# Performance work log

Measured on AMD Instinct MI355X. Metric: run time of the kernel, lower is better.

The kernel has to match this reference:

```python
import jax, jax.numpy as jnp
import numpy as np

B, S, D, H = 2, 2048, 2048, 16
HD = D // H  # 128 head dim


def setup_inputs() -> dict:
    key = jax.random.key(0)
    k1, k2, k3 = jax.random.split(key, 3)
    x = jax.random.normal(k1, (B, S, D), dtype=jnp.float32)
    w_qkv = jax.random.normal(k2, (3 * D, D), dtype=jnp.float32) * 0.02
    w_out = jax.random.normal(k3, (D, D), dtype=jnp.float32) * 0.02
    # complex-like RoPE table: freqs_cis[s, j] = exp(i * s * theta^{-2j/hd})
    theta = 10000.0
    inv_freq = 1.0 / (theta ** (jnp.arange(0, HD, 2, dtype=jnp.float32) / HD))  # [HD/2]
    t = jnp.arange(S, dtype=jnp.float32)
    freqs = jnp.outer(t, inv_freq)  # [S, HD/2]
    return {"x": x, "w_qkv": w_qkv, "w_out": w_out,
            "freqs_cos": jnp.cos(freqs), "freqs_sin": jnp.sin(freqs)}


def _apply_rope(t, cos, sin):
    # t: [b, s, h, hd]; adjacent pairs treated as complex (real, imag)
    b, s, h, hd = t.shape
    tr = t.reshape(b, s, h, hd // 2, 2)
    re, im = tr[..., 0], tr[..., 1]
    c = cos[None, :, None, :]  # [1, s, 1, hd/2]
    sn = sin[None, :, None, :]
    out_re = re * c - im * sn
    out_im = re * sn + im * c
    return jnp.stack([out_re, out_im], axis=-1).reshape(b, s, h, hd)


def reference(x, w_qkv, w_out, freqs_cos, freqs_sin):
    b, s, d = x.shape
    qkv = x @ w_qkv.T  # [b, s, 3d]
    q, k, v = jnp.split(qkv, 3, axis=-1)
    q = q.reshape(b, s, H, HD)
    k = k.reshape(b, s, H, HD)
    v = v.reshape(b, s, H, HD)
    q = _apply_rope(q, freqs_cos, freqs_sin)
    k = _apply_rope(k, freqs_cos, freqs_sin)
    # causal SDPA
    scale = 1.0 / jnp.sqrt(jnp.asarray(HD, dtype=x.dtype))
    scores = jnp.einsum("bqhd,bkhd->bhqk", q, k) * scale  # [b, h, s, s]
    causal = jnp.tril(jnp.ones((s, s), dtype=bool))
    scores = jnp.where(causal[None, None], scores, jnp.finfo(scores.dtype).min)
    attn = jax.nn.softmax(scores, axis=-1)
    out = jnp.einsum("bhqk,bkhd->bqhd", attn, v).reshape(b, s, d)
    return out @ w_out.T
```

## Files before the change

### kernel.cpp

```cpp
#include <hip/hip_runtime.h>
#include <hip/hip_bf16.h>
#include <stdint.h>

#define S_ 2048
#define D_ 2048
#define H_ 16
#define HD_ 128

typedef __bf16 bf16x8 __attribute__((ext_vector_type(8)));
typedef float f32x4 __attribute__((ext_vector_type(4)));
typedef unsigned short ushort_t;
typedef ushort_t us4 __attribute__((ext_vector_type(4)));

__device__ __forceinline__ float bf2f(ushort_t u) {
  union { float f; uint32_t i; } x; x.i = ((uint32_t)u) << 16; return x.f;
}
__device__ __forceinline__ ushort_t f2bf(float f) {
  union { float f; uint32_t i; } x; x.f = f;
  uint32_t r = x.i + 0x7fffu + ((x.i >> 16) & 1u);
  return (ushort_t)(r >> 16);
}

__device__ __forceinline__ void async_copy16(const void* g, void* l) {
  __builtin_amdgcn_global_load_lds(
      (const __attribute__((address_space(1))) unsigned int*)g,
      (__attribute__((address_space(3))) unsigned int*)l, 16, 0, 0);
}

__device__ __forceinline__ void store_val(float* p, float v) { *p = v; }
__device__ __forceinline__ void store_val(ushort_t* p, float v) { *p = f2bf(v); }

__global__ __launch_bounds__(256) void cvt_f32_bf16(const float* __restrict__ in,
                                                    ushort_t* __restrict__ out,
                                                    int n4) {
  int i = blockIdx.x * 256 + threadIdx.x;
  if (i >= n4) return;
  const float4 v = ((const float4*)in)[i];
  us4 o;
  o.x = f2bf(v.x); o.y = f2bf(v.y); o.z = f2bf(v.z); o.w = f2bf(v.w);
  ((us4*)out)[i] = o;
}

template <typename OutT>
__global__ __launch_bounds__(256) void gemm_bt(const ushort_t* __restrict__ A,
                                               const ushort_t* __restrict__ Bm,
                                               OutT* __restrict__ C,
                                               int M, int N, int K) {
  __shared__ __align__(16) ushort_t As[128 * 32];
  __shared__ __align__(16) ushort_t Bs[128 * 32];
  const int tid = threadIdx.x;
  const int wave = tid >> 6, lane = tid & 63;
  const int quad = lane >> 4, l16 = lane & 15;
  const int bm = blockIdx.y * 128, bn = blockIdx.x * 128;
  const int wm = (wave >> 1) * 64, wn = (wave & 1) * 64;

  f32x4 acc[4][4] = {};

  const int c0 = wave * 2, c1 = c0 + 1;
  const int srow = lane >> 2;
  const int scol = (lane & 3) * 8;
  const ushort_t* gA0 = A + (size_t)(bm + c0 * 16 + srow) * K + scol;
  const ushort_t* gA1 = A + (size_t)(bm + c1 * 16 + srow) * K + scol;
  const ushort_t* gB0 = Bm + (size_t)(bn + c0 * 16 + srow) * K + scol;
  const ushort_t* gB1 = Bm + (size_t)(bn + c1 * 16 + srow) * K + scol;
  ushort_t* lA0 = As + c0 * 512;
  ushort_t* lA1 = As + c1 * 512;
  ushort_t* lB0 = Bs + c0 * 512;
  ushort_t* lB1 = Bs + c1 * 512;

  for (int k0 = 0; k0 < K; k0 += 32) {
    __syncthreads();
    async_copy16(gA0 + k0, lA0);
    async_copy16(gA1 + k0, lA1);
    async_copy16(gB0 + k0, lB0);
    async_copy16(gB1 + k0, lB1);
    __syncthreads();
    bf16x8 af[4], bfr[4];
#pragma unroll
    for (int i = 0; i < 4; ++i)
      af[i] = *(const bf16x8*)(As + (wm + i * 16 + l16) * 32 + quad * 8);
#pragma unroll
    for (int i = 0; i < 4; ++i)
      bfr[i] = *(const bf16x8*)(Bs + (wn + i * 16 + l16) * 32 + quad * 8);
#pragma unroll
    for (int mi = 0; mi < 4; ++mi)
#pragma unroll
      for (int ni = 0; ni < 4; ++ni)
        acc[mi][ni] = __builtin_amdgcn_mfma_f32_16x16x32_bf16(af[mi], bfr[ni],
                                                              acc[mi][ni], 0, 0, 0);
  }
#pragma unroll
  for (int mi = 0; mi < 4; ++mi)
#pragma unroll
    for (int ni = 0; ni < 4; ++ni)
#pragma unroll
      for (int r = 0; r < 4; ++r) {
        int row = bm + wm + mi * 16 + quad * 4 + r;
        int col = bn + wn + ni * 16 + l16;
        store_val(&C[(size_t)row * N + col], acc[mi][ni][r]);
      }
}

__device__ __forceinline__ void stage_half(const ushort_t* __restrict__ g, int K,
                                           ushort_t* l, int wave, int srow,
                                           int clog) {
#pragma unroll
  for (int i = 0; i < 2; ++i)
    async_copy16(g + (size_t)(i * 64 + srow) * K + clog * 8,
                 l + wave * 512 + i * 4096);
}

#define MFMA_BF16(a, b, c) __builtin_amdgcn_mfma_f32_16x16x32_bf16(a, b, c, 0, 0, 0)

template <typename OutT>
__global__ __launch_bounds__(512, 2) void gemm_bt256(const ushort_t* __restrict__ A,
                                                     const ushort_t* __restrict__ Bm,
                                                     OutT* __restrict__ C,
                                                     int M, int N, int K) {
  __shared__ __align__(16) ushort_t As[2][256 * 64];
  __shared__ __align__(16) ushort_t Bs[2][256 * 64];
  const int tid = threadIdx.x;
  const int wave = tid >> 6, lane = tid & 63;
  const int quad = lane >> 4, l16 = lane & 15;
  const int bm = blockIdx.y * 256, bn = blockIdx.x * 256;
  const int wm = (wave >> 2) * 128;
  const int wn = (wave & 3) * 64;
  const int srow = tid >> 3;
  const int clog = (tid & 7) ^ (srow & 7);
  const int ck0 = (quad ^ (l16 & 7)) * 8;
  const int ck1 = ((4 + quad) ^ (l16 & 7)) * 8;

  const ushort_t* gA = A + (size_t)bm * K;
  const ushort_t* gB = Bm + (size_t)bn * K;
  const int NT = K >> 6;

  f32x4 acc[8][4] = {};

  const ushort_t* ArowE = &As[0][0] + (wm + l16) * 64;
  const ushort_t* BrowE = &Bs[0][0] + (wn + l16) * 64;
  const ushort_t* ArowO = &As[1][0] + (wm + l16) * 64;
  const ushort_t* BrowO = &Bs[1][0] + (wn + l16) * 64;

  stage_half(gB, K, &Bs[0][0], wave, srow, clog);
  stage_half(gB + (size_t)128 * K, K, &Bs[0][8192], wave, srow, clog);
  stage_half(gA, K, &As[0][0], wave, srow, clog);
  stage_half(gA + (size_t)128 * K, K, &As[0][8192], wave, srow, clog);
  stage_half(gB + 64, K, &Bs[1][0], wave, srow, clog);
  stage_half(gB + (size_t)128 * K + 64, K, &Bs[1][8192], wave, srow, clog);
  asm volatile("s_waitcnt vmcnt(4)" ::: "memory");
  __builtin_amdgcn_sched_barrier(0);
  __builtin_amdgcn_s_barrier();

  for (int ii = 0; ii < (NT >> 1); ++ii) {
    const int t = 2 * ii;
    const int t2 = (t + 2 < NT) ? t + 2 : NT - 1;
    const int t3 = (t + 3 < NT) ? t + 3 : NT - 1;
    const size_t k1 = (size_t)(t + 1) * 64;
    const size_t k2 = (size_t)t2 * 64;
    const size_t k3 = (size_t)t3 * 64;

    bf16x8 a4[4][2], b01[2][2], b23[2][2];

#pragma unroll
    for (int mi = 0; mi < 4; ++mi) {
      a4[mi][0] = *(const bf16x8*)(ArowE + mi * 1024 + ck0);
      a4[mi][1] = *(const bf16x8*)(ArowE + mi * 1024 + ck1);
    }
#pragma unroll
    for (int ni = 0; ni < 2; ++ni) {
      b01[ni][0] = *(const bf16x8*)(BrowE + ni * 1024 + ck0);
      b01[ni][1] = *(const bf16x8*)(BrowE + ni * 1024 + ck1);
    }
    stage_half(gA + k1, K, &As[1][0], wave, srow, clog);
    __builtin_amdgcn_s_barrier();
    __builtin_amdgcn_s_setprio(1);
#pragma unroll
    for (int ks = 0; ks < 2; ++ks)
#pragma unroll
      for (int mi = 0; mi < 4; ++mi)
#pragma unroll
        for (int ni = 0; ni < 2; ++ni)
          acc[mi][ni] = MFMA_BF16(a4[mi][ks], b01[ni][ks], acc[mi][ni]);
    __builtin_amdgcn_s_setprio(0);
    __builtin_amdgcn_s_barrier();

#pragma unroll
    for (int ni = 0; ni < 2; ++ni) {
      b23[ni][0] = *(const bf16x8*)(BrowE + (ni + 2) * 1024 + ck0);
      b23[ni][1] = *(const bf16x8*)(BrowE + (ni + 2) * 1024 + ck1);
    }
    stage_half(gA + (size_t)128 * K + k1, K, &As[1][8192], wave, srow, clog);
    __builtin_amdgcn_s_barrier();
    __builtin_amdgcn_s_setprio(1);
#pragma unroll
    for (int ks = 0; ks < 2; ++ks)
#pragma unroll
      for (int mi = 0; mi < 4; ++mi)
#pragma unroll
        for (int ni = 0; ni < 2; ++ni)
          acc[mi][ni + 2] = MFMA_BF16(a4[mi][ks], b23[ni][ks], acc[mi][ni + 2]);
    __builtin_amdgcn_s_setprio(0);
    __builtin_amdgcn_s_barrier();

#pragma unroll
    for (int mi = 0; mi < 4; ++mi) {
      a4[mi][0] = *(const bf16x8*)(ArowE + (mi + 4) * 1024 + ck0);
      a4[mi][1] = *(const bf16x8*)(ArowE + (mi + 4) * 1024 + ck1);
    }
    stage_half(gB + k2, K, &Bs[0][0], wave, srow, clog);
    __builtin_amdgcn_s_barrier();
    __builtin_amdgcn_s_setprio(1);
#pragma unroll
    for (int ks = 0; ks < 2; ++ks)
#pragma unroll
      for (int mi = 0; mi < 4; ++mi)
#pragma unroll
        for (int ni = 0; ni < 2; ++ni)
          acc[mi + 4][ni] = MFMA_BF16(a4[mi][ks], b01[ni][ks], acc[mi + 4][ni]);
    __builtin_amdgcn_s_setprio(0);
    __builtin_amdgcn_s_barrier();

    stage_half(gB + (size_t)128 * K + k2, K, &Bs[0][8192], wave, srow, clog);
    asm volatile("s_waitcnt vmcnt(4)" ::: "memory");
    __builtin_amdgcn_sched_barrier(0);
    __builtin_amdgcn_s_barrier();
    __builtin_amdgcn_s_setprio(1);
#pragma unroll
    for (int ks = 0; ks < 2; ++ks)
#pragma unroll
      for (int mi = 0; mi < 4; ++mi)
#pragma unroll
        for (int ni = 0; ni < 2; ++ni)
          acc[mi + 4][ni + 2] = MFMA_BF16(a4[mi][ks], b23[ni][ks], acc[mi + 4][ni + 2]);
    __builtin_amdgcn_s_setprio(0);
    __builtin_amdgcn_s_barrier();

#pragma unroll
    for (int mi = 0; mi < 4; ++mi) {
      a4[mi][0] = *(const bf16x8*)(ArowO + mi * 1024 + ck0);
      a4[mi][1] = *(const bf16x8*)(ArowO + mi * 1024 + ck1);
    }
#pragma unroll
    for (int ni = 0; ni < 2; ++ni) {
      b01[ni][0] = *(const bf16x8*)(BrowO + ni * 1024 + ck0);
      b01[ni][1] = *(const bf16x8*)(BrowO + ni * 1024 + ck1);
    }
    stage_half(gA + k2, K, &As[0][0], wave, srow, clog);
    __builtin_amdgcn_s_barrier();
    __builtin_amdgcn_s_setprio(1);
#pragma unroll
    for (int ks = 0; ks < 2; ++ks)
#pragma unroll
      for (int mi = 0; mi < 4; ++mi)
#pragma unroll
        for (int ni = 0; ni < 2; ++ni)
          acc[mi][ni] = MFMA_BF16(a4[mi][ks], b01[ni][ks], acc[mi][ni]);
    __builtin_amdgcn_s_setprio(0);
    __builtin_amdgcn_s_barrier();

#pragma unroll
    for (int ni = 0; ni < 2; ++ni) {
      b23[ni][0] = *(const bf16x8*)(BrowO + (ni + 2) * 1024 + ck0);
      b23[ni][1] = *(const bf16x8*)(BrowO + (ni + 2) * 1024 + ck1);
    }
    stage_half(gA + (size_t)128 * K + k2, K, &As[0][8192], wave, srow, clog);
    __builtin_amdgcn_s_barrier();
    __builtin_amdgcn_s_setprio(1);
#pragma unroll
    for (int ks = 0; ks < 2; ++ks)
#pragma unroll
      for (int mi = 0; mi < 4; ++mi)
#pragma unroll
        for (int ni = 0; ni < 2; ++ni)
          acc[mi][ni + 2] = MFMA_BF16(a4[mi][ks], b23[ni][ks], acc[mi][ni + 2]);
    __builtin_amdgcn_s_setprio(0);
    __builtin_amdgcn_s_barrier();

#pragma unroll
    for (int mi = 0; mi < 4; ++mi) {
      a4[mi][0] = *(const bf16x8*)(ArowO + (mi + 4) * 1024 + ck0);
      a4[mi][1] = *(const bf16x8*)(ArowO + (mi + 4) * 1024 + ck1);
    }
    stage_half(gB + k3, K, &Bs[1][0], wave, srow, clog);
    __builtin_amdgcn_s_barrier();
    __builtin_amdgcn_s_setprio(1);
#pragma unroll
    for (int ks = 0; ks < 2; ++ks)
#pragma unroll
      for (int mi = 0; mi < 4; ++mi)
#pragma unroll
        for (int ni = 0; ni < 2; ++ni)
          acc[mi + 4][ni] = MFMA_BF16(a4[mi][ks], b01[ni][ks], acc[mi + 4][ni]);
    __builtin_amdgcn_s_setprio(0);
    __builtin_amdgcn_s_barrier();

    stage_half(gB + (size_t)128 * K + k3, K, &Bs[1][8192], wave, srow, clog);
    asm volatile("s_waitcnt vmcnt(4)" ::: "memory");
    __builtin_amdgcn_sched_barrier(0);
    __builtin_amdgcn_s_barrier();
    __builtin_amdgcn_s_setprio(1);
#pragma unroll
    for (int ks = 0; ks < 2; ++ks)
#pragma unroll
      for (int mi = 0; mi < 4; ++mi)
#pragma unroll
        for (int ni = 0; ni < 2; ++ni)
          acc[mi + 4][ni + 2] = MFMA_BF16(a4[mi][ks], b23[ni][ks], acc[mi + 4][ni + 2]);
    __builtin_amdgcn_s_setprio(0);
    __builtin_amdgcn_s_barrier();
    __builtin_amdgcn_sched_barrier(0);
  }

  asm volatile("s_waitcnt vmcnt(0)" ::: "memory");

#pragma unroll
  for (int mi = 0; mi < 8; ++mi)
#pragma unroll
    for (int ni = 0; ni < 4; ++ni)
#pragma unroll
      for (int r = 0; r < 4; ++r) {
        int row = bm + wm + mi * 16 + quad * 4 + r;
        int col = bn + wn + ni * 16 + l16;
        store_val(&C[(size_t)row * N + col], acc[mi][ni][r]);
      }
}

__global__ __launch_bounds__(256) void rope_k(ushort_t* __restrict__ qkv,
                                              const float* __restrict__ fc,
                                              const float* __restrict__ fs) {
  int idx = blockIdx.x * 256 + threadIdx.x;
  int i = idx & 63;
  int hh = (idx >> 6) & 15;
  int m = idx >> 10;
  int s = m & (S_ - 1);
  float c = fc[s * 64 + i], sn = fs[s * 64 + i];
  size_t off = (size_t)m * (3 * D_) + hh * HD_ + 2 * i;
#pragma unroll
  for (int part = 0; part < 2; ++part) {
    uint32_t* p = (uint32_t*)(qkv + off + part * D_);
    uint32_t v = *p;
    float re = bf2f((ushort_t)(v & 0xffffu));
    float im = bf2f((ushort_t)(v >> 16));
    float nr = re * c - im * sn;
    float ni = re * sn + im * c;
    *p = (uint32_t)f2bf(nr) | ((uint32_t)f2bf(ni) << 16);
  }
}

__global__ __launch_bounds__(256) void vt_prep(const ushort_t* __restrict__ qkv,
                                               ushort_t* __restrict__ VTg) {
  __shared__ __align__(16) ushort_t T[64 * 136];
  const int st = blockIdx.x, h = blockIdx.y, b = blockIdx.z;
  const int tid = threadIdx.x;
  const ushort_t* gV = qkv + (size_t)(b * S_ + st * 64) * (3 * D_) + 2 * D_ + h * HD_;
  {
    const int r = tid >> 2, cc = (tid & 3) * 32;
    const ushort_t* src = gV + (size_t)r * (3 * D_) + cc;
    uint4 a0 = ((const uint4*)src)[0];
    uint4 a1 = ((const uint4*)src)[1];
    uint4 a2 = ((const uint4*)src)[2];
    uint4 a3 = ((const uint4*)src)[3];
    ushort_t* dst = T + r * 136 + cc;
    ((uint4*)dst)[0] = a0; ((uint4*)dst)[1] = a1;
    ((uint4*)dst)[2] = a2; ((uint4*)dst)[3] = a3;
  }
  __syncthreads();
  const int d = tid >> 1, kh = (tid & 1) * 32;
  ushort_t buf[32];
#pragma unroll
  for (int j = 0; j < 32; ++j) buf[j] = T[(kh + j) * 136 + d];
  ushort_t* out = VTg + ((size_t)((b * H_ + h) * HD_ + d)) * S_ + st * 64 + kh;
  ((uint4*)out)[0] = *(const uint4*)(buf + 0);
  ((uint4*)out)[1] = *(const uint4*)(buf + 8);
  ((uint4*)out)[2] = *(const uint4*)(buf + 16);
  ((uint4*)out)[3] = *(const uint4*)(buf + 24);
}

#define SOFTMAX_C 12.0f

__global__ __launch_bounds__(256, 4) void attn_fwd(const ushort_t* __restrict__ qkv,
                                                   const ushort_t* __restrict__ VTg,
                                                   float* __restrict__ Oacc,
                                                   float* __restrict__ lsum_g) {
  __shared__ __align__(16) ushort_t Kl[64 * 128];
  __shared__ __align__(16) ushort_t VT[128 * 64];
  __shared__ __align__(16) ushort_t Pl[4 * 16 * 64];

  const int j = 79 - (int)blockIdx.x;
  int qt, c;
  if (j < 8)       { qt = j;                 c = 0; }
  else if (j < 24) { int t = j - 8;  qt = 8 + (t >> 1);  c = t & 1; }
  else if (j < 48) { int t = j - 24; qt = 16 + t / 3;    c = t % 3; }
  else             { int t = j - 48; qt = 24 + (t >> 2); c = t & 3; }
  const int h = blockIdx.y, b = blockIdx.z;
  const int kt0 = c * 8;
  const int kt_end = min(kt0 + 8, qt + 1);

  const int tid = threadIdx.x;
  const int wave = tid >> 6, lane = tid & 63;
  const int quad = lane >> 4, l16 = lane & 15;
  const float scale = 0.08838834764831845f;

  const int qg = qt * 64 + wave * 16 + l16;
  const ushort_t* qrow = qkv + (size_t)(b * S_ + qg) * (3 * D_) + h * HD_;
  bf16x8 qf[4];
#pragma unroll
  for (int cc = 0; cc < 4; ++cc)
    qf[cc] = *(const bf16x8*)(qrow + cc * 32 + quad * 8);

  f32x4 o[8] = {};
  float lsum[4] = {0.f, 0.f, 0.f, 0.f};
  const int q_row_base = qt * 64 + wave * 16 + quad * 4;
  ushort_t* Pw = Pl + wave * 16 * 64;

  const ushort_t* gK = qkv + (size_t)(b * S_) * (3 * D_) + D_ + h * HD_;
  const ushort_t* gVT = VTg + (size_t)(b * H_ + h) * HD_ * S_;

  const int krow_off = lane >> 4;
  const int kchunk = lane & 15;
  const int vrow_off = lane >> 3;
  const int vchunk = lane & 7;

  for (int kt = kt0; kt < kt_end; ++kt) {
    __syncthreads();
#pragma unroll
    for (int i = 0; i < 4; ++i) {
      int row = wave * 16 + i * 4 + krow_off;
      int lchunk = kchunk ^ (row & 15);
      async_copy16(gK + (size_t)(kt * 64 + row) * (3 * D_) + lchunk * 8,
                   Kl + (wave * 16 + i * 4) * 128);
    }
#pragma unroll
    for (int i = 0; i < 4; ++i) {
      int row = wave * 32 + i * 8 + vrow_off;
      int lchunk = vchunk ^ (row & 7);
      async_copy16(gVT + (size_t)row * S_ + kt * 64 + lchunk * 8,
                   VT + (wave * 32 + i * 8) * 64);
    }
    __syncthreads();

    const bool diag = (kt == qt);
#pragma unroll
    for (int g = 0; g < 4; ++g) {
      f32x4 s = {0.f, 0.f, 0.f, 0.f};
#pragma unroll
      for (int cc = 0; cc < 4; ++cc) {
        bf16x8 kf = *(const bf16x8*)(Kl + (g * 16 + l16) * 128 +
                                     (((cc * 4 + quad) ^ l16) * 8));
        s = __builtin_amdgcn_mfma_f32_16x16x32_bf16(qf[cc], kf, s, 0, 0, 0);
      }
      const int key = kt * 64 + g * 16 + l16;
#pragma unroll
      for (int r = 0; r < 4; ++r) {
        float e = __expf(s[r] * scale - SOFTMAX_C);
        float p = (!diag || key <= q_row_base + r) ? e : 0.f;
        lsum[r] += p;
        int prow = quad * 4 + r;
        int pcol = g * 16 + l16;
        Pw[prow * 64 + (((pcol >> 3) ^ (prow & 7)) * 8) + (pcol & 7)] = f2bf(p);
      }
    }
    bf16x8 pf0 = *(const bf16x8*)(Pw + l16 * 64 + ((quad ^ (l16 & 7)) * 8));
    bf16x8 pf1 = *(const bf16x8*)(Pw + l16 * 64 + (((4 + quad) ^ (l16 & 7)) * 8));
#pragma unroll
    for (int dc = 0; dc < 8; ++dc) {
      bf16x8 v0 = *(const bf16x8*)(VT + (dc * 16 + l16) * 64 +
                                   (((0 * 4 + quad) ^ (l16 & 7)) * 8));
      o[dc] = __builtin_amdgcn_mfma_f32_16x16x32_bf16(pf0, v0, o[dc], 0, 0, 0);
      bf16x8 v1 = *(const bf16x8*)(VT + (dc * 16 + l16) * 64 +
                                   (((1 * 4 + quad) ^ (l16 & 7)) * 8));
      o[dc] = __builtin_amdgcn_mfma_f32_16x16x32_bf16(pf1, v1, o[dc], 0, 0, 0);
    }
  }

#pragma unroll
  for (int r = 0; r < 4; ++r) {
    float l = lsum[r];
    l += __shfl_xor(l, 1, 64);
    l += __shfl_xor(l, 2, 64);
    l += __shfl_xor(l, 4, 64);
    l += __shfl_xor(l, 8, 64);
    size_t row = (size_t)(b * S_ + q_row_base + r);
    if (l16 == 0) unsafeAtomicAdd(&lsum_g[row * H_ + h], l);
#pragma unroll
    for (int dc = 0; dc < 8; ++dc)
      unsafeAtomicAdd(&Oacc[row * D_ + h * HD_ + dc * 16 + l16], o[dc][r]);
  }
}

__global__ __launch_bounds__(256) void combine(const float* __restrict__ Oacc,
                                               const float* __restrict__ lsum_g,
                                               ushort_t* __restrict__ attn) {
  int i = blockIdx.x * 256 + threadIdx.x;
  float4 v = ((const float4*)Oacc)[i];
  int flat = i * 4;
  int row = flat >> 11;
  int h = (flat >> 7) & 15;
  float inv = 1.0f / lsum_g[row * H_ + h];
  us4 o;
  o.x = f2bf(v.x * inv); o.y = f2bf(v.y * inv);
  o.z = f2bf(v.z * inv); o.w = f2bf(v.w * inv);
  ((us4*)attn)[i] = o;
}

extern "C" void kernel_launch(void* const* d_in, const int* in_sizes, int n_in,
                              void* d_out, int out_size, void* d_ws, size_t ws_size,
                              hipStream_t stream) {
  const float* x = (const float*)d_in[0];
  const float* w_qkv = (const float*)d_in[1];
  const float* w_out = (const float*)d_in[2];
  const float* fcos = (const float*)d_in[3];
  const float* fsin = (const float*)d_in[4];
  float* out = (float*)d_out;

  char* ws = (char*)d_ws;
  ushort_t* x_bf    = (ushort_t*)(ws + 0);
  ushort_t* wqkv_bf = (ushort_t*)(ws + 16777216);
  ushort_t* wout_bf = (ushort_t*)(ws + 41943040);
  ushort_t* qkv     = (ushort_t*)(ws + 50331648);
  ushort_t* attn    = (ushort_t*)(ws + 100663296);
  float* Oacc   = (float*)(ws + 0);
  float* lsum_g = (float*)(ws + 33554432);
  ushort_t* VTg = (ushort_t*)(ws + 100663296);

  cvt_f32_bf16<<<8192, 256, 0, stream>>>(x, x_bf, 2097152);
  cvt_f32_bf16<<<12288, 256, 0, stream>>>(w_qkv, wqkv_bf, 3145728);
  cvt_f32_bf16<<<4096, 256, 0, stream>>>(w_out, wout_bf, 1048576);

  gemm_bt256<ushort_t><<<dim3(24, 16), 512, 0, stream>>>(x_bf, wqkv_bf, qkv,
                                                         4096, 6144, 2048);
  rope_k<<<16384, 256, 0, stream>>>(qkv, fcos, fsin);
  vt_prep<<<dim3(32, 16, 2), 256, 0, stream>>>(qkv, VTg);

  hipMemsetAsync(Oacc, 0, 33554432, stream);
  hipMemsetAsync(lsum_g, 0, 262144, stream);

  attn_fwd<<<dim3(80, 16, 2), 256, 0, stream>>>(qkv, VTg, Oacc, lsum_g);
  combine<<<8192, 256, 0, stream>>>(Oacc, lsum_g, attn);

  gemm_bt<float><<<dim3(16, 32), 256, 0, stream>>>(attn, wout_bf, out,
                                                   4096, 2048, 2048);
}
```

Measured before the change: 452.9 us.

## Use 128x256-tile pipelined GEMM for QKV and output projections

Replaces the 256x256 QKV GEMM with a 128x256 tile variant, which doubles the grid to 768 blocks for better CU fill. It also replaces the simple 128x128 single-buffered output-projection GEMM with the same double-buffered, swizzled, barrier-scheduled kernel. The out-projection should gain from LDS double buffering and larger tiles. The trade-offs are lower arithmetic intensity per block for the QKV GEMM and only 256 blocks for the output GEMM, which may underfill the 256 CUs.

```diff
diff --git a/kernel.cpp b/kernel.cpp
--- a/kernel.cpp
+++ b/kernel.cpp
@@ -41,66 +41,6 @@
   ((us4*)out)[i] = o;
 }
 
-template <typename OutT>
-__global__ __launch_bounds__(256) void gemm_bt(const ushort_t* __restrict__ A,
-                                               const ushort_t* __restrict__ Bm,
-                                               OutT* __restrict__ C,
-                                               int M, int N, int K) {
-  __shared__ __align__(16) ushort_t As[128 * 32];
-  __shared__ __align__(16) ushort_t Bs[128 * 32];
-  const int tid = threadIdx.x;
-  const int wave = tid >> 6, lane = tid & 63;
-  const int quad = lane >> 4, l16 = lane & 15;
-  const int bm = blockIdx.y * 128, bn = blockIdx.x * 128;
-  const int wm = (wave >> 1) * 64, wn = (wave & 1) * 64;
-
-  f32x4 acc[4][4] = {};
-
-  const int c0 = wave * 2, c1 = c0 + 1;
-  const int srow = lane >> 2;
-  const int scol = (lane & 3) * 8;
-  const ushort_t* gA0 = A + (size_t)(bm + c0 * 16 + srow) * K + scol;
-  const ushort_t* gA1 = A + (size_t)(bm + c1 * 16 + srow) * K + scol;
-  const ushort_t* gB0 = Bm + (size_t)(bn + c0 * 16 + srow) * K + scol;
-  const ushort_t* gB1 = Bm + (size_t)(bn + c1 * 16 + srow) * K + scol;
-  ushort_t* lA0 = As + c0 * 512;
-  ushort_t* lA1 = As + c1 * 512;
-  ushort_t* lB0 = Bs + c0 * 512;
-  ushort_t* lB1 = Bs + c1 * 512;
-
-  for (int k0 = 0; k0 < K; k0 += 32) {
-    __syncthreads();
-    async_copy16(gA0 + k0, lA0);
-    async_copy16(gA1 + k0, lA1);
-    async_copy16(gB0 + k0, lB0);
-    async_copy16(gB1 + k0, lB1);
-    __syncthreads();
-    bf16x8 af[4], bfr[4];
-#pragma unroll
-    for (int i = 0; i < 4; ++i)
-      af[i] = *(const bf16x8*)(As + (wm + i * 16 + l16) * 32 + quad * 8);
-#pragma unroll
-    for (int i = 0; i < 4; ++i)
-      bfr[i] = *(const bf16x8*)(Bs + (wn + i * 16 + l16) * 32 + quad * 8);
-#pragma unroll
-    for (int mi = 0; mi < 4; ++mi)
-#pragma unroll
-      for (int ni = 0; ni < 4; ++ni)
-        acc[mi][ni] = __builtin_amdgcn_mfma_f32_16x16x32_bf16(af[mi], bfr[ni],
-                                                              acc[mi][ni], 0, 0, 0);
-  }
-#pragma unroll
-  for (int mi = 0; mi < 4; ++mi)
-#pragma unroll
-    for (int ni = 0; ni < 4; ++ni)
-#pragma unroll
-      for (int r = 0; r < 4; ++r) {
-        int row = bm + wm + mi * 16 + quad * 4 + r;
-        int col = bn + wn + ni * 16 + l16;
-        store_val(&C[(size_t)row * N + col], acc[mi][ni][r]);
-      }
-}
-
 __device__ __forceinline__ void stage_half(const ushort_t* __restrict__ g, int K,
                                            ushort_t* l, int wave, int srow,
                                            int clog) {
@@ -113,17 +53,17 @@
 #define MFMA_BF16(a, b, c) __builtin_amdgcn_mfma_f32_16x16x32_bf16(a, b, c, 0, 0, 0)
 
 template <typename OutT>
-__global__ __launch_bounds__(512, 2) void gemm_bt256(const ushort_t* __restrict__ A,
-                                                     const ushort_t* __restrict__ Bm,
-                                                     OutT* __restrict__ C,
-                                                     int M, int N, int K) {
-  __shared__ __align__(16) ushort_t As[2][256 * 64];
+__global__ __launch_bounds__(512, 2) void gemm_bt128_256(const ushort_t* __restrict__ A,
+                                                         const ushort_t* __restrict__ Bm,
+                                                         OutT* __restrict__ C,
+                                                         int M, int N, int K) {
+  __shared__ __align__(16) ushort_t As[2][128 * 64];
   __shared__ __align__(16) ushort_t Bs[2][256 * 64];
   const int tid = threadIdx.x;
   const int wave = tid >> 6, lane = tid & 63;
   const int quad = lane >> 4, l16 = lane & 15;
-  const int bm = blockIdx.y * 256, bn = blockIdx.x * 256;
-  const int wm = (wave >> 2) * 128;
+  const int bm = blockIdx.y * 128, bn = blockIdx.x * 256;
+  const int wm = (wave >> 2) * 64;
   const int wn = (wave & 3) * 64;
   const int srow = tid >> 3;
   const int clog = (tid & 7) ^ (srow & 7);
@@ -134,17 +74,16 @@
   const ushort_t* gB = Bm + (size_t)bn * K;
   const int NT = K >> 6;
 
-  f32x4 acc[8][4] = {};
+  f32x4 acc[4][4] = {};
 
   const ushort_t* ArowE = &As[0][0] + (wm + l16) * 64;
   const ushort_t* BrowE = &Bs[0][0] + (wn + l16) * 64;
   const ushort_t* ArowO = &As[1][0] + (wm + l16) * 64;
   const ushort_t* BrowO = &Bs[1][0] + (wn + l16) * 64;
 
+  stage_half(gA, K, &As[0][0], wave, srow, clog);
   stage_half(gB, K, &Bs[0][0], wave, srow, clog);
   stage_half(gB + (size_t)128 * K, K, &Bs[0][8192], wave, srow, clog);
-  stage_half(gA, K, &As[0][0], wave, srow, clog);
-  stage_half(gA + (size_t)128 * K, K, &As[0][8192], wave, srow, clog);
   stage_half(gB + 64, K, &Bs[1][0], wave, srow, clog);
   stage_half(gB + (size_t)128 * K + 64, K, &Bs[1][8192], wave, srow, clog);
   asm volatile("s_waitcnt vmcnt(4)" ::: "memory");
@@ -162,7 +101,7 @@
     bf16x8 a4[4][2], b01[2][2], b23[2][2];
 
 #pragma unroll
-    for (int mi = 0; mi < 4; ++mi) {
+    for (int mi = 0; mi < 2; ++mi) {
       a4[mi][0] = *(const bf16x8*)(ArowE + mi * 1024 + ck0);
       a4[mi][1] = *(const bf16x8*)(ArowE + mi * 1024 + ck1);
     }
@@ -177,7 +116,7 @@
 #pragma unroll
     for (int ks = 0; ks < 2; ++ks)
 #pragma unroll
-      for (int mi = 0; mi < 4; ++mi)
+      for (int mi = 0; mi < 2; ++mi)
 #pragma unroll
         for (int ni = 0; ni < 2; ++ni)
           acc[mi][ni] = MFMA_BF16(a4[mi][ks], b01[ni][ks], acc[mi][ni]);
@@ -189,13 +128,12 @@
       b23[ni][0] = *(const bf16x8*)(BrowE + (ni + 2) * 1024 + ck0);
       b23[ni][1] = *(const bf16x8*)(BrowE + (ni + 2) * 1024 + ck1);
     }
-    stage_half(gA + (size_t)128 * K + k1, K, &As[1][8192], wave, srow, clog);
-    __builtin_amdgcn_s_barrier();
-    __builtin_amdgcn_s_setprio(1);
-#pragma unroll
-    for (int ks = 0; ks < 2; ++ks)
-#pragma unroll
-      for (int mi = 0; mi < 4; ++mi)
+    __builtin_amdgcn_s_barrier();
+    __builtin_amdgcn_s_setprio(1);
+#pragma unroll
+    for (int ks = 0; ks < 2; ++ks)
+#pragma unroll
+      for (int mi = 0; mi < 2; ++mi)
 #pragma unroll
         for (int ni = 0; ni < 2; ++ni)
           acc[mi][ni + 2] = MFMA_BF16(a4[mi][ks], b23[ni][ks], acc[mi][ni + 2]);
@@ -203,9 +141,9 @@
     __builtin_amdgcn_s_barrier();
 
 #pragma unroll
-    for (int mi = 0; mi < 4; ++mi) {
-      a4[mi][0] = *(const bf16x8*)(ArowE + (mi + 4) * 1024 + ck0);
-      a4[mi][1] = *(const bf16x8*)(ArowE + (mi + 4) * 1024 + ck1);
+    for (int mi = 0; mi < 2; ++mi) {
+      a4[mi + 2][0] = *(const bf16x8*)(ArowE + (mi + 2) * 1024 + ck0);
+      a4[mi + 2][1] = *(const bf16x8*)(ArowE + (mi + 2) * 1024 + ck1);
     }
     stage_half(gB + k2, K, &Bs[0][0], wave, srow, clog);
     __builtin_amdgcn_s_barrier();
@@ -213,10 +151,10 @@
 #pragma unroll
     for (int ks = 0; ks < 2; ++ks)
 #pragma unroll
-      for (int mi = 0; mi < 4; ++mi)
-#pragma unroll
-        for (int ni = 0; ni < 2; ++ni)
-          acc[mi + 4][ni] = MFMA_BF16(a4[mi][ks], b01[ni][ks], acc[mi + 4][ni]);
+      for (int mi = 0; mi < 2; ++mi)
+#pragma unroll
+        for (int ni = 0; ni < 2; ++ni)
+          acc[mi + 2][ni] = MFMA_BF16(a4[mi + 2][ks], b01[ni][ks], acc[mi + 2][ni]);
     __builtin_amdgcn_s_setprio(0);
     __builtin_amdgcn_s_barrier();
 
@@ -228,15 +166,15 @@
 #pragma unroll
     for (int ks = 0; ks < 2; ++ks)
 #pragma unroll
-      for (int mi = 0; mi < 4; ++mi)
-#pragma unroll
-        for (int ni = 0; ni < 2; ++ni)
-          acc[mi + 4][ni + 2] = MFMA_BF16(a4[mi][ks], b23[ni][ks], acc[mi + 4][ni + 2]);
-    __builtin_amdgcn_s_setprio(0);
-    __builtin_amdgcn_s_barrier();
-
-#pragma unroll
-    for (int mi = 0; mi < 4; ++mi) {
+      for (int mi = 0; mi < 2; ++mi)
+#pragma unroll
+        for (int ni = 0; ni < 2; ++ni)
+          acc[mi + 2][ni + 2] = MFMA_BF16(a4[mi + 2][ks], b23[ni][ks], acc[mi + 2][ni + 2]);
+    __builtin_amdgcn_s_setprio(0);
+    __builtin_amdgcn_s_barrier();
+
+#pragma unroll
+    for (int mi = 0; mi < 2; ++mi) {
       a4[mi][0] = *(const bf16x8*)(ArowO + mi * 1024 + ck0);
       a4[mi][1] = *(const bf16x8*)(ArowO + mi * 1024 + ck1);
     }
@@ -251,7 +189,7 @@
 #pragma unroll
     for (int ks = 0; ks < 2; ++ks)
 #pragma unroll
-      for (int mi = 0; mi < 4; ++mi)
+      for (int mi = 0; mi < 2; ++mi)
 #pragma unroll
         for (int ni = 0; ni < 2; ++ni)
           acc[mi][ni] = MFMA_BF16(a4[mi][ks], b01[ni][ks], acc[mi][ni]);
@@ -263,13 +201,12 @@
       b23[ni][0] = *(const bf16x8*)(BrowO + (ni + 2) * 1024 + ck0);
       b23[ni][1] = *(const bf16x8*)(BrowO + (ni + 2) * 1024 + ck1);
     }
-    stage_half(gA + (size_t)128 * K + k2, K, &As[0][8192], wave, srow, clog);
-    __builtin_amdgcn_s_barrier();
-    __builtin_amdgcn_s_setprio(1);
-#pragma unroll
-    for (int ks = 0; ks < 2; ++ks)
-#pragma unroll
-      for (int mi = 0; mi < 4; ++mi)
+    __builtin_amdgcn_s_barrier();
+    __builtin_amdgcn_s_setprio(1);
+#pragma unroll
+    for (int ks = 0; ks < 2; ++ks)
+#pragma unroll
+      for (int mi = 0; mi < 2; ++mi)
 #pragma unroll
         for (int ni = 0; ni < 2; ++ni)
           acc[mi][ni + 2] = MFMA_BF16(a4[mi][ks], b23[ni][ks], acc[mi][ni + 2]);
@@ -277,9 +214,9 @@
     __builtin_amdgcn_s_barrier();
 
 #pragma unroll
-    for (int mi = 0; mi < 4; ++mi) {
-      a4[mi][0] = *(const bf16x8*)(ArowO + (mi + 4) * 1024 + ck0);
-      a4[mi][1] = *(const bf16x8*)(ArowO + (mi + 4) * 1024 + ck1);
+    for (int mi = 0; mi < 2; ++mi) {
+      a4[mi + 2][0] = *(const bf16x8*)(ArowO + (mi + 2) * 1024 + ck0);
+      a4[mi + 2][1] = *(const bf16x8*)(ArowO + (mi + 2) * 1024 + ck1);
     }
     stage_half(gB + k3, K, &Bs[1][0], wave, srow, clog);
     __builtin_amdgcn_s_barrier();
@@ -287,10 +224,10 @@
 #pragma unroll
     for (int ks = 0; ks < 2; ++ks)
 #pragma unroll
-      for (int mi = 0; mi < 4; ++mi)
-#pragma unroll
-        for (int ni = 0; ni < 2; ++ni)
-          acc[mi + 4][ni] = MFMA_BF16(a4[mi][ks], b01[ni][ks], acc[mi + 4][ni]);
+      for (int mi = 0; mi < 2; ++mi)
+#pragma unroll
+        for (int ni = 0; ni < 2; ++ni)
+          acc[mi + 2][ni] = MFMA_BF16(a4[mi + 2][ks], b01[ni][ks], acc[mi + 2][ni]);
     __builtin_amdgcn_s_setprio(0);
     __builtin_amdgcn_s_barrier();
 
@@ -302,10 +239,10 @@
 #pragma unroll
     for (int ks = 0; ks < 2; ++ks)
 #pragma unroll
-      for (int mi = 0; mi < 4; ++mi)
-#pragma unroll
-        for (int ni = 0; ni < 2; ++ni)
-          acc[mi + 4][ni + 2] = MFMA_BF16(a4[mi][ks], b23[ni][ks], acc[mi + 4][ni + 2]);
+      for (int mi = 0; mi < 2; ++mi)
+#pragma unroll
+        for (int ni = 0; ni < 2; ++ni)
+          acc[mi + 2][ni + 2] = MFMA_BF16(a4[mi + 2][ks], b23[ni][ks], acc[mi + 2][ni + 2]);
     __builtin_amdgcn_s_setprio(0);
     __builtin_amdgcn_s_barrier();
     __builtin_amdgcn_sched_barrier(0);
@@ -314,7 +251,7 @@
   asm volatile("s_waitcnt vmcnt(0)" ::: "memory");
 
 #pragma unroll
-  for (int mi = 0; mi < 8; ++mi)
+  for (int mi = 0; mi < 4; ++mi)
 #pragma unroll
     for (int ni = 0; ni < 4; ++ni)
 #pragma unroll
@@ -527,8 +464,8 @@
   cvt_f32_bf16<<<12288, 256, 0, stream>>>(w_qkv, wqkv_bf, 3145728);
   cvt_f32_bf16<<<4096, 256, 0, stream>>>(w_out, wout_bf, 1048576);
 
-  gemm_bt256<ushort_t><<<dim3(24, 16), 512, 0, stream>>>(x_bf, wqkv_bf, qkv,
-                                                         4096, 6144, 2048);
+  gemm_bt128_256<ushort_t><<<dim3(24, 32), 512, 0, stream>>>(x_bf, wqkv_bf, qkv,
+                                                             4096, 6144, 2048);
   rope_k<<<16384, 256, 0, stream>>>(qkv, fcos, fsin);
   vt_prep<<<dim3(32, 16, 2), 256, 0, stream>>>(qkv, VTg);
 
@@ -538,6 +475,6 @@
   attn_fwd<<<dim3(80, 16, 2), 256, 0, stream>>>(qkv, VTg, Oacc, lsum_g);
   combine<<<8192, 256, 0, stream>>>(Oacc, lsum_g, attn);
 
-  gemm_bt<float><<<dim3(16, 32), 256, 0, stream>>>(attn, wout_bf, out,
-                                                   4096, 2048, 2048);
-}
+  gemm_bt128_256<float><<<dim3(8, 32), 512, 0, stream>>>(attn, wout_bf, out,
+                                                         4096, 2048, 2048);
+}
```

After: 446.2 us. Within noise of the previous version (-1.5%).
